# Performance work log

Measured on AMD Instinct MI355X. Metric: run time of the kernel, lower is better.

The kernel has to match this reference:

```python
import jax, jax.numpy as jnp
import numpy as np

N = 50000   # nodes per sample
H = 5000    # hyperedges
E = 400000  # incidence entries
B = 2       # batch
C = 64      # channels (in == out, heads = 1)
NEG_SLOPE = 0.2


def setup_inputs() -> dict:
    key = jax.random.key(0)
    k1, k2, k3, k4, k5 = jax.random.split(key, 5)
    x = jax.random.normal(k1, (B, N, C), jnp.float32)
    # glorot-ish scales for params
    weight = jax.random.normal(k2, (C, C), jnp.float32) * (1.0 / np.sqrt(C))
    att = jax.random.normal(k3, (1, 1, 2 * C), jnp.float32) * 0.1
    node_idx = jax.random.randint(k4, (E,), 0, N)
    # sorted so hyperedge ids appear in order (matches dict insertion order in source)
    hedge_idx = jnp.sort(jax.random.randint(k5, (E,), 0, H))
    return {"x": x, "weight": weight, "att": att,
            "node_idx": node_idx, "hedge_idx": hedge_idx}


def reference(x, weight, att, node_idx, hedge_idx):
    # x: [B,N,C] -> project and move node dim first: x1 [N,B,C]
    xw = jnp.einsum('bnc,cd->bnd', x, weight)
    x1 = jnp.transpose(xw, (1, 0, 2))

    xi = x1[node_idx]  # gather per incidence: [E,B,C]
    # per-hyperedge sum of member node features (the dict loop in source)
    edge_sums = jax.ops.segment_sum(xi, hedge_idx, num_segments=H)  # [H,B,C]
    xj = edge_sums[hedge_idx]  # [E,B,C]

    # attention logits: ([E,B,2C] * att[1,1,2C]).sum(-1) -> [E,B]
    alpha = (jnp.concatenate([xi, xj], axis=-1) * att).sum(-1)
    alpha = jnp.where(alpha >= 0, alpha, NEG_SLOPE * alpha)  # leaky_relu

    # segment softmax over node ids (num_nodes = N), stable
    seg_max = jax.ops.segment_max(alpha, node_idx, num_segments=N)
    seg_max = jnp.where(jnp.isfinite(seg_max), seg_max, 0.0)
    ex = jnp.exp(alpha - seg_max[node_idx])
    denom = jax.ops.segment_sum(ex, node_idx, num_segments=N)
    alpha = ex / denom[node_idx]  # [E,B]; dropout is identity in eval

    ones = jnp.ones((node_idx.shape[0],), x.dtype)
    Dn = jax.ops.segment_sum(ones, node_idx, num_segments=N)   # node degree (NOT inverted in source)
    De = jax.ops.segment_sum(ones, hedge_idx, num_segments=H)
    Binv = jnp.where(De > 0, 1.0 / De, 0.0)                    # 1/deg, inf -> 0

    # pass 1 (source_to_target): nodes -> hyperedges, norm = Binv[edge]
    m = jax.ops.segment_sum(Binv[hedge_idx][:, None, None] * alpha[:, :, None] * xi,
                            hedge_idx, num_segments=H)          # [H,B,C]
    # pass 2 (target_to_source): hyperedges -> nodes, norm = Dn[node]
    out = jax.ops.segment_sum(Dn[node_idx][:, None, None] * alpha[:, :, None] * m[hedge_idx],
                              node_idx, num_segments=N)         # [N,B,C]
    return jnp.transpose(out, (1, 0, 2))  # [B,N,C]
```

## Files before the change

kernel.cpp:

```cpp
#include <hip/hip_runtime.h>
#include <math.h>

#define N_NODES 50000
#define N_HEDGE 5000
#define N_EDGES 400000
#define NB 2
#define NC 64
#define NEG 0.2f
#define NROWS (N_NODES * NB)
#define MAXDEG 64

#define SCAT_BLOCKS ((N_EDGES + 255) / 256)
#define HEDGE_BLOCKS ((N_HEDGE + 3) / 4)

__device__ __forceinline__ unsigned short f2bf(float f) {
    unsigned int u = __float_as_uint(f);
    unsigned int r = (u + 0x7FFFu + ((u >> 16) & 1u)) >> 16;
    return (unsigned short)r;
}

__device__ __forceinline__ float lrelu_exp(float r) {
    r = (r >= 0.f) ? r : NEG * r;
    r = fmaxf(r, -80.f);
    return __expf(r);
}

__global__ __launch_bounds__(256, 4) void gemm_kernel(const float* __restrict__ x,
                                                      const float* __restrict__ W,
                                                      const float* __restrict__ att,
                                                      const int* __restrict__ node_idx,
                                                      const int* __restrict__ hedge_idx,
                                                      unsigned short* __restrict__ xwb,
                                                      float* __restrict__ p1,
                                                      float* __restrict__ p2,
                                                      int* __restrict__ cnt,
                                                      int* __restrict__ rank,
                                                      int* __restrict__ estart)
{
    __shared__ float xs[64 * 68];
    __shared__ float Ws[64 * 68];
    int t = threadIdx.x;
    int R = blockIdx.x * 64;

#pragma unroll
    for (int i = 0; i < 4; i++) {
        int lin = t + 256 * i;
        int r = lin >> 4, c4 = lin & 15;
        float4 wv = ((const float4*)W)[lin];
        *(float4*)&Ws[r * 68 + c4 * 4] = wv;
        int g = R + r;
        float4 xv = make_float4(0.f, 0.f, 0.f, 0.f);
        if (g < NROWS) {
            int n = g >> 1, b = g & 1;
            xv = ((const float4*)(x + ((size_t)b * N_NODES + n) * NC))[c4];
        }
        *(float4*)&xs[r * 68 + c4 * 4] = xv;
    }
    __syncthreads();

    int tr = t >> 4, tc = t & 15;
    float acc[4][4];
#pragma unroll
    for (int i = 0; i < 4; i++)
#pragma unroll
        for (int j = 0; j < 4; j++) acc[i][j] = 0.f;

#pragma unroll 4
    for (int k4 = 0; k4 < 16; k4++) {
        float4 xv[4], wv[4];
#pragma unroll
        for (int i = 0; i < 4; i++)
            xv[i] = *(const float4*)&xs[(tr * 4 + i) * 68 + k4 * 4];
#pragma unroll
        for (int kk = 0; kk < 4; kk++)
            wv[kk] = *(const float4*)&Ws[(k4 * 4 + kk) * 68 + tc * 4];
#pragma unroll
        for (int i = 0; i < 4; i++) {
            acc[i][0] = fmaf(xv[i].x, wv[0].x, acc[i][0]);
            acc[i][1] = fmaf(xv[i].x, wv[0].y, acc[i][1]);
            acc[i][2] = fmaf(xv[i].x, wv[0].z, acc[i][2]);
            acc[i][3] = fmaf(xv[i].x, wv[0].w, acc[i][3]);
            acc[i][0] = fmaf(xv[i].y, wv[1].x, acc[i][0]);
            acc[i][1] = fmaf(xv[i].y, wv[1].y, acc[i][1]);
            acc[i][2] = fmaf(xv[i].y, wv[1].z, acc[i][2]);
            acc[i][3] = fmaf(xv[i].y, wv[1].w, acc[i][3]);
            acc[i][0] = fmaf(xv[i].z, wv[2].x, acc[i][0]);
            acc[i][1] = fmaf(xv[i].z, wv[2].y, acc[i][1]);
            acc[i][2] = fmaf(xv[i].z, wv[2].z, acc[i][2]);
            acc[i][3] = fmaf(xv[i].z, wv[2].w, acc[i][3]);
            acc[i][0] = fmaf(xv[i].w, wv[3].x, acc[i][0]);
            acc[i][1] = fmaf(xv[i].w, wv[3].y, acc[i][1]);
            acc[i][2] = fmaf(xv[i].w, wv[3].z, acc[i][2]);
            acc[i][3] = fmaf(xv[i].w, wv[3].w, acc[i][3]);
        }
    }

    float a1x = att[tc * 4], a1y = att[tc * 4 + 1], a1z = att[tc * 4 + 2], a1w = att[tc * 4 + 3];
    float a2x = att[64 + tc * 4], a2y = att[64 + tc * 4 + 1], a2z = att[64 + tc * 4 + 2], a2w = att[64 + tc * 4 + 3];
#pragma unroll
    for (int i = 0; i < 4; i++) {
        int g = R + tr * 4 + i;
        if (g < NROWS) {
            ushort4 bv;
            bv.x = f2bf(acc[i][0]); bv.y = f2bf(acc[i][1]);
            bv.z = f2bf(acc[i][2]); bv.w = f2bf(acc[i][3]);
            ((ushort4*)(xwb + (size_t)g * 64))[tc] = bv;
        }
        float v1 = acc[i][0] * a1x + acc[i][1] * a1y + acc[i][2] * a1z + acc[i][3] * a1w;
        float v2 = acc[i][0] * a2x + acc[i][1] * a2y + acc[i][2] * a2z + acc[i][3] * a2w;
#pragma unroll
        for (int off = 8; off >= 1; off >>= 1) {
            v1 += __shfl_xor(v1, off, 64);
            v2 += __shfl_xor(v2, off, 64);
        }
        if (tc == 0 && g < NROWS) { p1[g] = v1; p2[g] = v2; }
    }

    int gid = blockIdx.x * 256 + t;
    if (gid < N_EDGES) {
        rank[gid] = atomicAdd(&cnt[node_idx[gid]], 1);
    }
    if (gid <= N_HEDGE) {
        int lo = 0, hi = N_EDGES;
        while (lo < hi) {
            int mid = (lo + hi) >> 1;
            if (hedge_idx[mid] < gid) lo = mid + 1; else hi = mid;
        }
        estart[gid] = lo;
    }
}

__global__ __launch_bounds__(256) void sh_kernel(const int* __restrict__ node_idx,
                                                 const int* __restrict__ hedge_idx,
                                                 const int* __restrict__ rank,
                                                 int* __restrict__ hperm,
                                                 const float* __restrict__ p2,
                                                 const int* __restrict__ estart,
                                                 float* __restrict__ s2)
{
    if (blockIdx.x < SCAT_BLOCKS) {
        int e = blockIdx.x * 256 + threadIdx.x;
        if (e >= N_EDGES) return;
        int n = node_idx[e];
        int r = rank[e];
        if (r < MAXDEG) hperm[(n << 6) + r] = hedge_idx[e];
    } else {
        int wv = (blockIdx.x - SCAT_BLOCKS) * 4 + (threadIdx.x >> 6);
        if (wv >= N_HEDGE) return;
        int lane = threadIdx.x & 63;
        int s = estart[wv], e1 = estart[wv + 1];
        float a0 = 0.f, a1 = 0.f;
        for (int e = s + lane; e < e1; e += 128) {
            int eB = e + 64; bool vB = eB < e1;
            int nA = node_idx[e];
            int nB = node_idx[vB ? eB : s];
            float2 pA = ((const float2*)p2)[nA];
            float2 pB = ((const float2*)p2)[nB];
            a0 += pA.x + (vB ? pB.x : 0.f);
            a1 += pA.y + (vB ? pB.y : 0.f);
        }
#pragma unroll
        for (int off = 32; off >= 1; off >>= 1) {
            a0 += __shfl_xor(a0, off, 64);
            a1 += __shfl_xor(a1, off, 64);
        }
        if (lane == 0) { s2[wv * 2] = a0; s2[wv * 2 + 1] = a1; }
    }
}

__global__ __launch_bounds__(256) void den_kernel(const int* __restrict__ cnt,
                                                  const int* __restrict__ hperm,
                                                  const float* __restrict__ p1,
                                                  const float* __restrict__ s2,
                                                  float* __restrict__ den)
{
    int t = threadIdx.x;
    int n = blockIdx.x * 32 + (t >> 3);
    if (n >= N_NODES) return;
    int sub = t & 7;
    int s = n << 6;
    int d = cnt[n]; if (d > MAXDEG) d = MAXDEG;
    int e1 = s + d;
    float2 pn = ((const float2*)p1)[n];
    const float2* s2v = (const float2*)s2;
    float a0 = 0.f, a1 = 0.f;
    for (int j = s + sub; j < e1; j += 8) {
        float2 v = s2v[hperm[j]];
        a0 += lrelu_exp(pn.x + v.x);
        a1 += lrelu_exp(pn.y + v.y);
    }
#pragma unroll
    for (int off = 1; off < 8; off <<= 1) {
        a0 += __shfl_xor(a0, off, 64);
        a1 += __shfl_xor(a1, off, 64);
    }
    if (sub == 0) ((float2*)den)[n] = make_float2(a0, a1);
}

__global__ __launch_bounds__(256) void m_kernel(const unsigned short* __restrict__ xwb,
                                                const int* __restrict__ node_idx,
                                                const int* __restrict__ estart,
                                                const float* __restrict__ p1,
                                                const float* __restrict__ s2,
                                                const float* __restrict__ den,
                                                float* __restrict__ m)
{
    __shared__ float red[3][128];
    int h = blockIdx.x;
    int t = threadIdx.x;
    int w = t >> 6, l = t & 63;
    int g = l >> 4;
    int i = l & 15;
    int b = i >> 3;
    int s = estart[h], e1 = estart[h + 1];
    float2 s2h = ((const float2*)s2)[h];
    float sb = b ? s2h.y : s2h.x;

    float c0 = 0.f, c1 = 0.f, c2 = 0.f, c3 = 0.f;
    float c4 = 0.f, c5 = 0.f, c6 = 0.f, c7 = 0.f;

    for (int eb = s + 4 * w; eb < e1; eb += 64) {
        int eA = eb + g;      bool vA = eA < e1;
        int eB = eb + 16 + g; bool vB = eB < e1;
        int eC = eb + 32 + g; bool vC = eC < e1;
        int eD = eb + 48 + g; bool vD = eD < e1;
        int nA = node_idx[vA ? eA : s];
        int nB = node_idx[vB ? eB : s];
        int nC = node_idx[vC ? eC : s];
        int nD = node_idx[vD ? eD : s];
        float pA = p1[2 * nA + b], pB = p1[2 * nB + b];
        float pC = p1[2 * nC + b], pD = p1[2 * nD + b];
        float dA = den[2 * nA + b], dB = den[2 * nB + b];
        float dC = den[2 * nC + b], dD = den[2 * nD + b];
        uint4 qA = *(const uint4*)&xwb[(size_t)nA * 128 + 8 * i];
        uint4 qB = *(const uint4*)&xwb[(size_t)nB * 128 + 8 * i];
        uint4 qC = *(const uint4*)&xwb[(size_t)nC * 128 + 8 * i];
        uint4 qD = *(const uint4*)&xwb[(size_t)nD * 128 + 8 * i];

        float aA = lrelu_exp(pA + sb) * __builtin_amdgcn_rcpf(dA); aA = vA ? aA : 0.f;
        float aB = lrelu_exp(pB + sb) * __builtin_amdgcn_rcpf(dB); aB = vB ? aB : 0.f;
        float aC = lrelu_exp(pC + sb) * __builtin_amdgcn_rcpf(dC); aC = vC ? aC : 0.f;
        float aD = lrelu_exp(pD + sb) * __builtin_amdgcn_rcpf(dD); aD = vD ? aD : 0.f;

        c0 = fmaf(aA, __uint_as_float(qA.x << 16), c0);
        c1 = fmaf(aA, __uint_as_float(qA.x & 0xffff0000u), c1);
        c2 = fmaf(aA, __uint_as_float(qA.y << 16), c2);
        c3 = fmaf(aA, __uint_as_float(qA.y & 0xffff0000u), c3);
        c4 = fmaf(aA, __uint_as_float(qA.z << 16), c4);
        c5 = fmaf(aA, __uint_as_float(qA.z & 0xffff0000u), c5);
        c6 = fmaf(aA, __uint_as_float(qA.w << 16), c6);
        c7 = fmaf(aA, __uint_as_float(qA.w & 0xffff0000u), c7);
        c0 = fmaf(aB, __uint_as_float(qB.x << 16), c0);
        c1 = fmaf(aB, __uint_as_float(qB.x & 0xffff0000u), c1);
        c2 = fmaf(aB, __uint_as_float(qB.y << 16), c2);
        c3 = fmaf(aB, __uint_as_float(qB.y & 0xffff0000u), c3);
        c4 = fmaf(aB, __uint_as_float(qB.z << 16), c4);
        c5 = fmaf(aB, __uint_as_float(qB.z & 0xffff0000u), c5);
        c6 = fmaf(aB, __uint_as_float(qB.w << 16), c6);
        c7 = fmaf(aB, __uint_as_float(qB.w & 0xffff0000u), c7);
        c0 = fmaf(aC, __uint_as_float(qC.x << 16), c0);
        c1 = fmaf(aC, __uint_as_float(qC.x & 0xffff0000u), c1);
        c2 = fmaf(aC, __uint_as_float(qC.y << 16), c2);
        c3 = fmaf(aC, __uint_as_float(qC.y & 0xffff0000u), c3);
        c4 = fmaf(aC, __uint_as_float(qC.z << 16), c4);
        c5 = fmaf(aC, __uint_as_float(qC.z & 0xffff0000u), c5);
        c6 = fmaf(aC, __uint_as_float(qC.w << 16), c6);
        c7 = fmaf(aC, __uint_as_float(qC.w & 0xffff0000u), c7);
        c0 = fmaf(aD, __uint_as_float(qD.x << 16), c0);
        c1 = fmaf(aD, __uint_as_float(qD.x & 0xffff0000u), c1);
        c2 = fmaf(aD, __uint_as_float(qD.y << 16), c2);
        c3 = fmaf(aD, __uint_as_float(qD.y & 0xffff0000u), c3);
        c4 = fmaf(aD, __uint_as_float(qD.z << 16), c4);
        c5 = fmaf(aD, __uint_as_float(qD.z & 0xffff0000u), c5);
        c6 = fmaf(aD, __uint_as_float(qD.w << 16), c6);
        c7 = fmaf(aD, __uint_as_float(qD.w & 0xffff0000u), c7);
    }

#pragma unroll
    for (int off = 16; off <= 32; off <<= 1) {
        c0 += __shfl_xor(c0, off, 64);
        c1 += __shfl_xor(c1, off, 64);
        c2 += __shfl_xor(c2, off, 64);
        c3 += __shfl_xor(c3, off, 64);
        c4 += __shfl_xor(c4, off, 64);
        c5 += __shfl_xor(c5, off, 64);
        c6 += __shfl_xor(c6, off, 64);
        c7 += __shfl_xor(c7, off, 64);
    }
    if (w && l < 16) {
        float* r = &red[w - 1][8 * l];
        r[0] = c0; r[1] = c1; r[2] = c2; r[3] = c3;
        r[4] = c4; r[5] = c5; r[6] = c6; r[7] = c7;
    }
    __syncthreads();
    if (w == 0 && l < 16) {
#pragma unroll
        for (int k = 0; k < 3; k++) {
            const float* r = &red[k][8 * l];
            c0 += r[0]; c1 += r[1]; c2 += r[2]; c3 += r[3];
            c4 += r[4]; c5 += r[5]; c6 += r[6]; c7 += r[7];
        }
        int d = e1 - s;
        float binv = (d > 0) ? 1.0f / (float)d : 0.0f;
        float* dst = m + (size_t)h * 128 + 8 * l;
        *(float4*)dst = make_float4(binv * c0, binv * c1, binv * c2, binv * c3);
        *(float4*)(dst + 4) = make_float4(binv * c4, binv * c5, binv * c6, binv * c7);
    }
}

__global__ __launch_bounds__(256) void out_kernel(const float* __restrict__ m,
                                                  const int* __restrict__ hperm,
                                                  const float* __restrict__ p1,
                                                  const float* __restrict__ s2,
                                                  const int* __restrict__ cnt,
                                                  float* __restrict__ out)
{
    int n = blockIdx.x * 4 + (threadIdx.x >> 6);
    if (n >= N_NODES) return;
    int l = threadIdx.x & 63;
    int g = l >> 5;
    int i = l & 31;
    int b = i >> 4;
    int d = cnt[n]; if (d > MAXDEG) d = MAXDEG;
    int s = n << 6;
    int e1 = s + d;
    float pnb = p1[2 * n + b];
    const float2* s2v = (const float2*)s2;
    float c0 = 0.f, c1 = 0.f, c2 = 0.f, c3 = 0.f, sden = 0.f;

    for (int jb = s; jb < e1; jb += 8) {
        int jA = jb + g;     bool vA = jA < e1;
        int jB = jb + 2 + g; bool vB = jB < e1;
        int jC = jb + 4 + g; bool vC = jC < e1;
        int jD = jb + 6 + g; bool vD = jD < e1;
        int hA = hperm[vA ? jA : s];
        int hB = hperm[vB ? jB : s];
        int hC = hperm[vC ? jC : s];
        int hD = hperm[vD ? jD : s];
        float2 wA = s2v[hA], wB = s2v[hB], wC = s2v[hC], wD = s2v[hD];
        float4 mA = *(const float4*)(m + (size_t)hA * 128 + 4 * i);
        float4 mB = *(const float4*)(m + (size_t)hB * 128 + 4 * i);
        float4 mC = *(const float4*)(m + (size_t)hC * 128 + 4 * i);
        float4 mD = *(const float4*)(m + (size_t)hD * 128 + 4 * i);
        float aA = lrelu_exp(pnb + (b ? wA.y : wA.x)); aA = vA ? aA : 0.f;
        float aB = lrelu_exp(pnb + (b ? wB.y : wB.x)); aB = vB ? aB : 0.f;
        float aC = lrelu_exp(pnb + (b ? wC.y : wC.x)); aC = vC ? aC : 0.f;
        float aD = lrelu_exp(pnb + (b ? wD.y : wD.x)); aD = vD ? aD : 0.f;
        sden += ((aA + aB) + aC) + aD;
        c0 = fmaf(aA, mA.x, c0); c1 = fmaf(aA, mA.y, c1);
        c2 = fmaf(aA, mA.z, c2); c3 = fmaf(aA, mA.w, c3);
        c0 = fmaf(aB, mB.x, c0); c1 = fmaf(aB, mB.y, c1);
        c2 = fmaf(aB, mB.z, c2); c3 = fmaf(aB, mB.w, c3);
        c0 = fmaf(aC, mC.x, c0); c1 = fmaf(aC, mC.y, c1);
        c2 = fmaf(aC, mC.z, c2); c3 = fmaf(aC, mC.w, c3);
        c0 = fmaf(aD, mD.x, c0); c1 = fmaf(aD, mD.y, c1);
        c2 = fmaf(aD, mD.z, c2); c3 = fmaf(aD, mD.w, c3);
    }
    c0 += __shfl_xor(c0, 32, 64);
    c1 += __shfl_xor(c1, 32, 64);
    c2 += __shfl_xor(c2, 32, 64);
    c3 += __shfl_xor(c3, 32, 64);
    sden += __shfl_xor(sden, 32, 64);
    if (l < 32) {
        float scale = (d > 0) ? (float)d * __builtin_amdgcn_rcpf(sden) : 0.f;
        int c = (4 * i) & 63;
        float* dst = out + (size_t)b * N_NODES * 64 + (size_t)n * 64 + c;
        __builtin_nontemporal_store(scale * c0, &dst[0]);
        __builtin_nontemporal_store(scale * c1, &dst[1]);
        __builtin_nontemporal_store(scale * c2, &dst[2]);
        __builtin_nontemporal_store(scale * c3, &dst[3]);
    }
}

extern "C" void kernel_launch(void* const* d_in, const int* in_sizes, int n_in,
                              void* d_out, int out_size, void* d_ws, size_t ws_size,
                              hipStream_t stream)
{
    const float* x      = (const float*)d_in[0];
    const float* W      = (const float*)d_in[1];
    const float* att    = (const float*)d_in[2];
    const int* node_idx = (const int*)d_in[3];
    const int* hedge_idx= (const int*)d_in[4];
    float* out = (float*)d_out;

    unsigned short* xwb = (unsigned short*)d_ws;
    float* p1     = (float*)(xwb + (size_t)NROWS * NC);
    float* p2     = p1 + NROWS;
    float* s2     = p2 + NROWS;
    float* m      = s2 + 10000;
    float* den    = m + (size_t)N_HEDGE * NB * NC;
    int* estart  = (int*)(den + NROWS);
    int* cnt     = estart + 5008;
    int* rank    = cnt + N_NODES;
    int* hperm   = rank + N_EDGES;

    hipMemsetAsync(cnt, 0, (size_t)N_NODES * sizeof(int), stream);

    gemm_kernel<<<(NROWS + 63) / 64, 256, 0, stream>>>(x, W, att, node_idx, hedge_idx,
                                                       xwb, p1, p2, cnt, rank, estart);
    sh_kernel<<<SCAT_BLOCKS + HEDGE_BLOCKS, 256, 0, stream>>>(node_idx, hedge_idx, rank,
                                                              hperm, p2, estart, s2);
    den_kernel<<<(N_NODES + 31) / 32, 256, 0, stream>>>(cnt, hperm, p1, s2, den);
    m_kernel<<<N_HEDGE, 256, 0, stream>>>(xwb, node_idx, estart, p1, s2, den, m);
    out_kernel<<<(N_NODES + 3) / 4, 256, 0, stream>>>(m, hperm, p1, s2, cnt, out);
}
```

Measured before the change: 162.1 us.

## Enlarge GEMM row tile to 128 and issue degree-count atomics before compute

The projection GEMM now covers 128 rows per block, with each thread accumulating 8 rows instead of 4, so every W value read from shared memory is reused across more rows. The launch is halved and each thread handles two incidence entries for the node-degree atomic counting. Those atomics are issued before the FMA loop so their latency can overlap with compute. The shared-memory pitch drops from 68 to 66, which leaves float4 LDS accesses only 8-byte aligned on odd rows, and the larger tile raises register pressure (launch bounds lowered to 3 blocks).

New measurement: 162.5 us. About the same (+0.2%).

```diff
diff --git a/kernel.cpp b/kernel.cpp
--- a/kernel.cpp
+++ b/kernel.cpp
@@ -10,8 +10,11 @@
 #define NROWS (N_NODES * NB)
 #define MAXDEG 64
 
+#define GEMM_BLOCKS ((NROWS + 127) / 128)
+#define GEMM_THREADS (GEMM_BLOCKS * 256)
 #define SCAT_BLOCKS ((N_EDGES + 255) / 256)
 #define HEDGE_BLOCKS ((N_HEDGE + 3) / 4)
+#define PITCH 66
 
 __device__ __forceinline__ unsigned short f2bf(float f) {
     unsigned int u = __float_as_uint(f);
@@ -25,7 +28,7 @@
     return __expf(r);
 }
 
-__global__ __launch_bounds__(256, 4) void gemm_kernel(const float* __restrict__ x,
+__global__ __launch_bounds__(256, 3) void gemm_kernel(const float* __restrict__ x,
                                                       const float* __restrict__ W,
                                                       const float* __restrict__ att,
                                                       const int* __restrict__ node_idx,
@@ -37,45 +40,66 @@
                                                       int* __restrict__ rank,
                                                       int* __restrict__ estart)
 {
-    __shared__ float xs[64 * 68];
-    __shared__ float Ws[64 * 68];
+    __shared__ float xs[128 * PITCH];
+    __shared__ float Ws[64 * PITCH];
     int t = threadIdx.x;
-    int R = blockIdx.x * 64;
-
-#pragma unroll
-    for (int i = 0; i < 4; i++) {
-        int lin = t + 256 * i;
-        int r = lin >> 4, c4 = lin & 15;
-        float4 wv = ((const float4*)W)[lin];
-        *(float4*)&Ws[r * 68 + c4 * 4] = wv;
-        int g = R + r;
-        float4 xv = make_float4(0.f, 0.f, 0.f, 0.f);
-        if (g < NROWS) {
-            int n = g >> 1, b = g & 1;
-            xv = ((const float4*)(x + ((size_t)b * N_NODES + n) * NC))[c4];
-        }
-        *(float4*)&xs[r * 68 + c4 * 4] = xv;
-    }
+    int R = blockIdx.x * 128;
+    int tq = t >> 4, tc = t & 15;
+
+    float4 w0 = ((const float4*)W)[t];
+    float4 w1 = ((const float4*)W)[t + 256];
+    float4 w2 = ((const float4*)W)[t + 512];
+    float4 w3 = ((const float4*)W)[t + 768];
+    float4 x0, x1, x2, x3, x4, x5, x6, x7;
+    {
+        float4 z = make_float4(0.f, 0.f, 0.f, 0.f);
+        x0 = z; x1 = z; x2 = z; x3 = z; x4 = z; x5 = z; x6 = z; x7 = z;
+#define LOADX(idx, dst) { int g = R + tq + 16 * idx;                                   \
+        if (g < NROWS) { int n = g >> 1, b = g & 1;                                    \
+            dst = ((const float4*)(x + ((size_t)b * N_NODES + n) * NC))[tc]; } }
+        LOADX(0, x0) LOADX(1, x1) LOADX(2, x2) LOADX(3, x3)
+        LOADX(4, x4) LOADX(5, x5) LOADX(6, x6) LOADX(7, x7)
+#undef LOADX
+    }
+    *(float4*)&Ws[(tq +  0) * PITCH + tc * 4] = w0;
+    *(float4*)&Ws[(tq + 16) * PITCH + tc * 4] = w1;
+    *(float4*)&Ws[(tq + 32) * PITCH + tc * 4] = w2;
+    *(float4*)&Ws[(tq + 48) * PITCH + tc * 4] = w3;
+    *(float4*)&xs[(tq +   0) * PITCH + tc * 4] = x0;
+    *(float4*)&xs[(tq +  16) * PITCH + tc * 4] = x1;
+    *(float4*)&xs[(tq +  32) * PITCH + tc * 4] = x2;
+    *(float4*)&xs[(tq +  48) * PITCH + tc * 4] = x3;
+    *(float4*)&xs[(tq +  64) * PITCH + tc * 4] = x4;
+    *(float4*)&xs[(tq +  80) * PITCH + tc * 4] = x5;
+    *(float4*)&xs[(tq +  96) * PITCH + tc * 4] = x6;
+    *(float4*)&xs[(tq + 112) * PITCH + tc * 4] = x7;
     __syncthreads();
 
-    int tr = t >> 4, tc = t & 15;
-    float acc[4][4];
-#pragma unroll
-    for (int i = 0; i < 4; i++)
+    int gid = blockIdx.x * 256 + t;
+    int gid2 = gid + GEMM_THREADS;
+    bool v2 = gid2 < N_EDGES;
+    int rk0 = atomicAdd(&cnt[node_idx[gid]], 1);
+    int rk1 = 0;
+    if (v2) rk1 = atomicAdd(&cnt[node_idx[gid2]], 1);
+
+    float acc[8][4];
+#pragma unroll
+    for (int i = 0; i < 8; i++)
 #pragma unroll
         for (int j = 0; j < 4; j++) acc[i][j] = 0.f;
 
 #pragma unroll 4
     for (int k4 = 0; k4 < 16; k4++) {
-        float4 xv[4], wv[4];
-#pragma unroll
-        for (int i = 0; i < 4; i++)
-            xv[i] = *(const float4*)&xs[(tr * 4 + i) * 68 + k4 * 4];
+        float4 wv[4];
 #pragma unroll
         for (int kk = 0; kk < 4; kk++)
-            wv[kk] = *(const float4*)&Ws[(k4 * 4 + kk) * 68 + tc * 4];
-#pragma unroll
-        for (int i = 0; i < 4; i++) {
+            wv[kk] = *(const float4*)&Ws[(k4 * 4 + kk) * PITCH + tc * 4];
+        float4 xv[8];
+#pragma unroll
+        for (int i = 0; i < 8; i++)
+            xv[i] = *(const float4*)&xs[(tq * 8 + i) * PITCH + k4 * 4];
+#pragma unroll
+        for (int i = 0; i < 8; i++) {
             acc[i][0] = fmaf(xv[i].x, wv[0].x, acc[i][0]);
             acc[i][1] = fmaf(xv[i].x, wv[0].y, acc[i][1]);
             acc[i][2] = fmaf(xv[i].x, wv[0].z, acc[i][2]);
@@ -98,8 +122,8 @@
     float a1x = att[tc * 4], a1y = att[tc * 4 + 1], a1z = att[tc * 4 + 2], a1w = att[tc * 4 + 3];
     float a2x = att[64 + tc * 4], a2y = att[64 + tc * 4 + 1], a2z = att[64 + tc * 4 + 2], a2w = att[64 + tc * 4 + 3];
 #pragma unroll
-    for (int i = 0; i < 4; i++) {
-        int g = R + tr * 4 + i;
+    for (int i = 0; i < 8; i++) {
+        int g = R + tq * 8 + i;
         if (g < NROWS) {
             ushort4 bv;
             bv.x = f2bf(acc[i][0]); bv.y = f2bf(acc[i][1]);
@@ -107,19 +131,17 @@
             ((ushort4*)(xwb + (size_t)g * 64))[tc] = bv;
         }
         float v1 = acc[i][0] * a1x + acc[i][1] * a1y + acc[i][2] * a1z + acc[i][3] * a1w;
-        float v2 = acc[i][0] * a2x + acc[i][1] * a2y + acc[i][2] * a2z + acc[i][3] * a2w;
+        float v2r = acc[i][0] * a2x + acc[i][1] * a2y + acc[i][2] * a2z + acc[i][3] * a2w;
 #pragma unroll
         for (int off = 8; off >= 1; off >>= 1) {
             v1 += __shfl_xor(v1, off, 64);
-            v2 += __shfl_xor(v2, off, 64);
-        }
-        if (tc == 0 && g < NROWS) { p1[g] = v1; p2[g] = v2; }
-    }
-
-    int gid = blockIdx.x * 256 + t;
-    if (gid < N_EDGES) {
-        rank[gid] = atomicAdd(&cnt[node_idx[gid]], 1);
-    }
+            v2r += __shfl_xor(v2r, off, 64);
+        }
+        if (tc == 0 && g < NROWS) { p1[g] = v1; p2[g] = v2r; }
+    }
+
+    rank[gid] = rk0;
+    if (v2) rank[gid2] = rk1;
     if (gid <= N_HEDGE) {
         int lo = 0, hi = N_EDGES;
         while (lo < hi) {
@@ -396,8 +418,8 @@
 
     hipMemsetAsync(cnt, 0, (size_t)N_NODES * sizeof(int), stream);
 
-    gemm_kernel<<<(NROWS + 63) / 64, 256, 0, stream>>>(x, W, att, node_idx, hedge_idx,
-                                                       xwb, p1, p2, cnt, rank, estart);
+    gemm_kernel<<<GEMM_BLOCKS, 256, 0, stream>>>(x, W, att, node_idx, hedge_idx,
+                                                 xwb, p1, p2, cnt, rank, estart);
     sh_kernel<<<SCAT_BLOCKS + HEDGE_BLOCKS, 256, 0, stream>>>(node_idx, hedge_idx, rank,
                                                               hperm, p2, estart, s2);
     den_kernel<<<(N_NODES + 31) / 32, 256, 0, stream>>>(cnt, hperm, p1, s2, den);
```
